# Optimization experiments

Measured on AMD Instinct MI355X. Metric: run time of the kernel, lower is better.

The kernel has to match this reference:

```python
import jax, jax.numpy as jnp
import numpy as np

L, D = 8192, 1024


def binary_operator_diag(q_i, q_j):
    # elementwise (diagonal) linear-recurrence combine: h_j = A_j * h_i + b_j
    A_i, b_i = q_i
    A_j, b_j = q_j
    return A_j * A_i, A_j * b_i + b_j


def setup_inputs() -> dict:
    key = jax.random.key(0)
    k_in, k_u, k_th, k_bre, k_bim = jax.random.split(key, 5)
    inputs = jax.random.normal(k_in, (L, D), dtype=jnp.float32)
    # stable LRU init: |lambda| = exp(-exp(nu)) = sqrt(u), u in (0.01, 0.99)
    u = jax.random.uniform(k_u, (D,), jnp.float32, 0.01, 0.99)
    nu = jnp.log(-0.5 * jnp.log(u))
    # phase stored in log-space (forward uses exp(theta))
    theta = jnp.log(jax.random.uniform(k_th, (D,), jnp.float32, 1e-3, 6.28))
    gamma_log = 0.5 * jnp.log(1.0 - u)  # = log(sqrt(1 - |lambda|^2))
    norm = np.float32(np.sqrt(2.0 * D))
    B_re = jax.random.normal(k_bre, (D, D), jnp.float32) / norm
    B_im = jax.random.normal(k_bim, (D, D), jnp.float32) / norm
    return {"inputs": inputs, "theta": theta, "nu": nu,
            "gamma_log": gamma_log, "B_re": B_re, "B_im": B_im}


def reference(inputs, theta, nu, gamma_log, B_re, B_im):
    # diagonal transition: lambda = exp(-exp(nu) + i*exp(theta)), shape [D]
    diag_lambda = jnp.exp(-jnp.exp(nu) + 1j * jnp.exp(theta))
    # normalized input matrix: (B_re + i B_im) * exp(gamma_log)[:, None]
    B_norm = (B_re + 1j * B_im) * jnp.exp(gamma_log)[:, None]  # [D, D] complex
    # Bu[t] = B_norm @ u_t  -> batched as one GEMM: [L, D] complex
    Bu = jnp.einsum('ld,kd->lk', inputs.astype(B_norm.dtype), B_norm)
    Lambda_elements = jnp.broadcast_to(diag_lambda[None, :], Bu.shape)
    # parallel associative scan over time (axis 0), elementwise over channels
    _, hidden_states = jax.lax.associative_scan(
        binary_operator_diag, (Lambda_elements, Bu))
    return hidden_states.real + inputs
```

## Files before the change

kernel.cpp:

```cpp
#include <hip/hip_runtime.h>
#include <cstdint>
#include <cstddef>

typedef float  f32x4   __attribute__((ext_vector_type(4)));
typedef short  bf16x8  __attribute__((ext_vector_type(8)));
typedef unsigned short u16x8 __attribute__((ext_vector_type(8)));

#define L_SEQ   8192
#define D_DIM   1024
#define N_COL   2048
#define N_PAIR  512
#define CHUNK_T 16
#define N_CHUNK 512

__device__ __forceinline__ unsigned short f2bf(float f) {
  unsigned int b = __float_as_uint(f);
  b += 0x7FFFu + ((b >> 16) & 1u);
  return (unsigned short)(b >> 16);
}
__device__ __forceinline__ float bf2f(unsigned short u) {
  return __uint_as_float((unsigned int)u << 16);
}
__device__ __forceinline__ void gload_lds16(const void* g, void* lds) {
  __builtin_amdgcn_global_load_lds(
      (const __attribute__((address_space(1))) void*)g,
      (__attribute__((address_space(3))) void*)lds, 16, 0, 0);
}
__device__ __forceinline__ float2 cmul(float2 a, float2 b) {
  return make_float2(a.x * b.x - a.y * b.y, a.x * b.y + a.y * b.x);
}
__device__ __forceinline__ float2 csqr(float2 a) {
  return make_float2(a.x * a.x - a.y * a.y, 2.f * a.x * a.y);
}
__device__ __forceinline__ void cfma2(const float4& lm, float2& h0, float2& h1,
                                      const float4& v) {
  float nr0 = fmaf(lm.x, h0.x, fmaf(-lm.y, h0.y, v.x));
  float ni0 = fmaf(lm.x, h0.y, fmaf(lm.y, h0.x, v.y));
  float nr1 = fmaf(lm.z, h1.x, fmaf(-lm.w, h1.y, v.z));
  float ni1 = fmaf(lm.z, h1.y, fmaf(lm.w, h1.x, v.w));
  h0.x = nr0; h0.y = ni0; h1.x = nr1; h1.y = ni1;
}

__global__ __launch_bounds__(256) void k_prep(
    const float* __restrict__ in, const float* __restrict__ Bre,
    const float* __restrict__ Bim, const float* __restrict__ gamma_log,
    const float* __restrict__ theta, const float* __restrict__ nu,
    unsigned short* __restrict__ A, unsigned short* __restrict__ W,
    float2* __restrict__ lam) {
  int b = blockIdx.x;
  if (b < 4096) {
    int i = b * 256 + threadIdx.x;
    const float4* p = (const float4*)in;
    float4 a = p[2 * i], c = p[2 * i + 1];
    u16x8 o;
    o[0] = f2bf(a.x); o[1] = f2bf(a.y); o[2] = f2bf(a.z); o[3] = f2bf(a.w);
    o[4] = f2bf(c.x); o[5] = f2bf(c.y); o[6] = f2bf(c.z); o[7] = f2bf(c.w);
    *(u16x8*)(A + (size_t)i * 8) = o;
  } else if (b < 5120) {
    int t = (b - 4096) * 256 + threadIdx.x;
    int row = t >> 7;
    int seg = t & 127;
    int k = row >> 1;
    const float* src = (row & 1) ? Bim : Bre;
    float g = expf(gamma_log[k]);
    const float4* p = (const float4*)(src + (size_t)k * D_DIM + seg * 8);
    float4 a = p[0], c = p[1];
    u16x8 o;
    o[0] = f2bf(a.x * g); o[1] = f2bf(a.y * g); o[2] = f2bf(a.z * g); o[3] = f2bf(a.w * g);
    o[4] = f2bf(c.x * g); o[5] = f2bf(c.y * g); o[6] = f2bf(c.z * g); o[7] = f2bf(c.w * g);
    *(u16x8*)(W + (size_t)row * D_DIM + seg * 8) = o;
  } else {
    int k = (b - 5120) * 256 + threadIdx.x;
    if (k < D_DIM) {
      float mod = expf(-expf(nu[k]));
      float ang = expf(theta[k]);
      lam[k] = make_float2(mod * cosf(ang), mod * sinf(ang));
    }
  }
}

__global__ __launch_bounds__(512, 1) void k_gemm(const unsigned short* __restrict__ A,
                                                 const unsigned short* __restrict__ W,
                                                 unsigned short* __restrict__ Bu16,
                                                 float2* __restrict__ agg2,
                                                 const float2* __restrict__ lam) {
  extern __shared__ char smem[];

  const int tid = threadIdx.x;
  const int l = tid & 63, w = tid >> 6;
  const int wm = w >> 2, wn = w & 3;

  int orig = blockIdx.x;
  int wgid = (orig & 7) * 32 + (orig >> 3);
  const int mt = wgid >> 3, nt = wgid & 7;
  const size_t m0 = (size_t)mt * 256, n0 = (size_t)nt * 256;

  const int srow = tid >> 3;
  const int scs  = tid & 7;
  const int cA   = scs ^ (srow & 7);
  const size_t srcoff0 = (size_t)srow * 2048 + (size_t)cA * 16;
  const size_t srcoff1 = srcoff0 + 64 * 2048;
  const int dst0 = tid * 16, dst1 = 8192 + tid * 16;

#define STAGE(Mptr, Mbase, Msel, bb, hh, TT) do {                                   \
    const char* s_ = (const char*)(Mptr) +                                          \
        (((Mbase) + (size_t)(hh) * 128) * 2048 + (size_t)(TT) * 128);               \
    char* d_ = smem + (Msel) * 65536 + (bb) * 32768 + (hh) * 16384;                 \
    gload_lds16(s_ + srcoff0, d_ + dst0);                                           \
    gload_lds16(s_ + srcoff1, d_ + dst1);                                           \
  } while (0)

  int aroff[8], broff[4];
#pragma unroll
  for (int fr = 0; fr < 8; ++fr) {
    int lrow = fr * 32 + wm * 16 + (l & 15);
    aroff[fr] = (lrow >> 7) * 16384 + (lrow & 127) * 128;
  }
#pragma unroll
  for (int fn = 0; fn < 4; ++fn) {
    int lrow = fn * 64 + wn * 16 + (l & 15);
    broff[fn] = (lrow >> 7) * 16384 + (lrow & 127) * 128;
  }
  const int swk0 = (((l >> 4)) ^ (l & 7)) << 4;
  const int swk1 = ((4 + (l >> 4)) ^ (l & 7)) << 4;

  f32x4 acc[8][4];
#pragma unroll
  for (int m = 0; m < 8; ++m)
#pragma unroll
    for (int n = 0; n < 4; ++n) acc[m][n] = (f32x4){0.f, 0.f, 0.f, 0.f};

  bf16x8 af[4][2], bfr[4][2];

#define LGKMC0 asm volatile("s_waitcnt lgkmcnt(0)" ::: "memory")
#define VMCNT4 asm volatile("s_waitcnt vmcnt(4)" ::: "memory")
#define VMCNT0 asm volatile("s_waitcnt vmcnt(0)" ::: "memory")
#define BAR()  do { asm volatile("" ::: "memory"); __builtin_amdgcn_s_barrier(); \
                    asm volatile("" ::: "memory"); } while (0)

  STAGE(W, n0, 1, 0, 0, 0);
  STAGE(A, m0, 0, 0, 1, 0);
  STAGE(A, m0, 0, 0, 0, 0);
  STAGE(W, n0, 1, 0, 1, 0);
  STAGE(W, n0, 1, 1, 0, 1);
  STAGE(A, m0, 0, 1, 1, 1);
  VMCNT4;
  BAR();

  for (int kt = 0; kt < 16; ++kt) {
    const int buf = kt & 1;
    const int abase = buf * 32768;
    const int bbase = 65536 + buf * 32768;
    const int b1 = (kt + 1) & 1, b2 = kt & 1;
    const bool s1 = (kt + 1 < 16), s2 = (kt + 2 < 16);

#pragma unroll
    for (int i = 0; i < 4; ++i) {
      af[i][0] = *(const bf16x8*)(smem + abase + aroff[i] + swk0);
      af[i][1] = *(const bf16x8*)(smem + abase + aroff[i] + swk1);
    }
#pragma unroll
    for (int fn = 0; fn < 2; ++fn) {
      bfr[fn][0] = *(const bf16x8*)(smem + bbase + broff[fn] + swk0);
      bfr[fn][1] = *(const bf16x8*)(smem + bbase + broff[fn] + swk1);
    }
    if (s1) STAGE(A, m0, 0, b1, 0, kt + 1);
    BAR();
    LGKMC0;
    __builtin_amdgcn_s_setprio(1);
#pragma unroll
    for (int i = 0; i < 4; ++i)
#pragma unroll
      for (int fn = 0; fn < 2; ++fn) {
        acc[i][fn] = __builtin_amdgcn_mfma_f32_16x16x32_bf16(af[i][0], bfr[fn][0], acc[i][fn], 0, 0, 0);
        acc[i][fn] = __builtin_amdgcn_mfma_f32_16x16x32_bf16(af[i][1], bfr[fn][1], acc[i][fn], 0, 0, 0);
      }
    __builtin_amdgcn_s_setprio(0);
    BAR();

#pragma unroll
    for (int fn = 2; fn < 4; ++fn) {
      bfr[fn][0] = *(const bf16x8*)(smem + bbase + broff[fn] + swk0);
      bfr[fn][1] = *(const bf16x8*)(smem + bbase + broff[fn] + swk1);
    }
    if (s1) STAGE(W, n0, 1, b1, 1, kt + 1);
    BAR();
    LGKMC0;
    __builtin_amdgcn_s_setprio(1);
#pragma unroll
    for (int i = 0; i < 4; ++i)
#pragma unroll
      for (int fn = 2; fn < 4; ++fn) {
        acc[i][fn] = __builtin_amdgcn_mfma_f32_16x16x32_bf16(af[i][0], bfr[fn][0], acc[i][fn], 0, 0, 0);
        acc[i][fn] = __builtin_amdgcn_mfma_f32_16x16x32_bf16(af[i][1], bfr[fn][1], acc[i][fn], 0, 0, 0);
      }
    __builtin_amdgcn_s_setprio(0);
    BAR();

#pragma unroll
    for (int i = 0; i < 4; ++i) {
      af[i][0] = *(const bf16x8*)(smem + abase + aroff[4 + i] + swk0);
      af[i][1] = *(const bf16x8*)(smem + abase + aroff[4 + i] + swk1);
    }
    if (s2) STAGE(W, n0, 1, b2, 0, kt + 2);
    BAR();
    LGKMC0;
    __builtin_amdgcn_s_setprio(1);
#pragma unroll
    for (int i = 0; i < 4; ++i)
#pragma unroll
      for (int fn = 2; fn < 4; ++fn) {
        acc[4 + i][fn] = __builtin_amdgcn_mfma_f32_16x16x32_bf16(af[i][0], bfr[fn][0], acc[4 + i][fn], 0, 0, 0);
        acc[4 + i][fn] = __builtin_amdgcn_mfma_f32_16x16x32_bf16(af[i][1], bfr[fn][1], acc[4 + i][fn], 0, 0, 0);
      }
    __builtin_amdgcn_s_setprio(0);
    BAR();

    if (s2) STAGE(A, m0, 0, b2, 1, kt + 2);
    __builtin_amdgcn_s_setprio(1);
#pragma unroll
    for (int i = 0; i < 4; ++i)
#pragma unroll
      for (int fn = 0; fn < 2; ++fn) {
        acc[4 + i][fn] = __builtin_amdgcn_mfma_f32_16x16x32_bf16(af[i][0], bfr[fn][0], acc[4 + i][fn], 0, 0, 0);
        acc[4 + i][fn] = __builtin_amdgcn_mfma_f32_16x16x32_bf16(af[i][1], bfr[fn][1], acc[4 + i][fn], 0, 0, 0);
      }
    __builtin_amdgcn_s_setprio(0);
    if (kt < 14) VMCNT4; else VMCNT0;
    BAR();
  }
#undef STAGE

#pragma unroll
  for (int fr = 0; fr < 8; ++fr)
#pragma unroll
    for (int fn = 0; fn < 4; ++fn) {
      int col = fn * 64 + wn * 16 + (l & 15);
#pragma unroll
      for (int j = 0; j < 4; ++j) {
        int row = fr * 32 + wm * 16 + (l >> 4) * 4 + j;
        int byte = row * 512 + ((col * 2) ^ ((row & 7) << 4));
        *(unsigned short*)(smem + byte) = f2bf(acc[fr][fn][j]);
      }
    }
  __syncthreads();

  {
    unsigned short* gbase = Bu16 + m0 * N_COL + n0;
#pragma unroll
    for (int pass = 0; pass < 16; ++pass) {
      int row = pass * 16 + (tid >> 5);
      int c = tid & 31;
      int byte = row * 512 + ((c * 16) ^ ((row & 7) << 4));
      f32x4 v = *(const f32x4*)(smem + byte);
      *(f32x4*)(gbase + (size_t)row * N_COL + c * 8) = v;
    }
  }

#pragma unroll
  for (int i = 0; i < 4; ++i) {
    int q = i * 512 + tid;
    int c = q >> 7, ch = q & 127;
    float2 lmv = lam[(n0 >> 1) + ch];
    unsigned int pr[16];
#pragma unroll
    for (int s = 0; s < 16; ++s) {
      int row = c * 16 + s;
      pr[s] = *(const unsigned int*)(smem + row * 512 + ((ch * 4) ^ ((row & 7) << 4)));
    }
    float2 h = {0.f, 0.f};
#pragma unroll
    for (int s = 0; s < 16; ++s) {
      float br = bf2f((unsigned short)(pr[s] & 0xFFFFu));
      float bi = bf2f((unsigned short)(pr[s] >> 16));
      float nr = fmaf(lmv.x, h.x, fmaf(-lmv.y, h.y, br));
      float ni = fmaf(lmv.x, h.y, fmaf(lmv.y, h.x, bi));
      h.x = nr; h.y = ni;
    }
    agg2[(size_t)(mt * 16 + c) * 1024 + (n0 >> 1) + ch] = h;
  }
}

__global__ __launch_bounds__(256) void k_scan2(const float4* __restrict__ agg4,
                                               const float4* __restrict__ lam4,
                                               float4* __restrict__ carry4) {
  int wave = blockIdx.x * 4 + (threadIdx.x >> 6);
  int lane = threadIdx.x & 63;
  int j = wave;
  float4 lm = lam4[j];
  float2 lT0 = {lm.x, lm.y}, lT1 = {lm.z, lm.w};
#pragma unroll
  for (int i = 0; i < 4; ++i) { lT0 = csqr(lT0); lT1 = csqr(lT1); }

  float4 a[8];
  float2 T0 = {0.f, 0.f}, T1 = {0.f, 0.f};
  float4 lTv = make_float4(lT0.x, lT0.y, lT1.x, lT1.y);
#pragma unroll
  for (int i = 0; i < 8; ++i) {
    a[i] = agg4[(size_t)(lane * 8 + i) * N_PAIR + j];
    cfma2(lTv, T0, T1, a[i]);
  }

  float2 M0 = lT0, M1 = lT1;
#pragma unroll
  for (int i = 0; i < 3; ++i) { M0 = csqr(M0); M1 = csqr(M1); }
  float2 S0 = T0, S1 = T1;
#pragma unroll
  for (int d = 1; d < 64; d <<= 1) {
    float2 u0, u1;
    u0.x = __shfl_up(S0.x, d); u0.y = __shfl_up(S0.y, d);
    u1.x = __shfl_up(S1.x, d); u1.y = __shfl_up(S1.y, d);
    if (lane >= d) {
      float2 m0 = cmul(M0, u0), m1 = cmul(M1, u1);
      S0.x += m0.x; S0.y += m0.y; S1.x += m1.x; S1.y += m1.y;
    }
    M0 = csqr(M0); M1 = csqr(M1);
  }
  float2 P0, P1;
  P0.x = __shfl_up(S0.x, 1); P0.y = __shfl_up(S0.y, 1);
  P1.x = __shfl_up(S1.x, 1); P1.y = __shfl_up(S1.y, 1);
  if (lane == 0) { P0 = make_float2(0.f, 0.f); P1 = make_float2(0.f, 0.f); }

#pragma unroll
  for (int i = 0; i < 8; ++i) {
    carry4[(size_t)(lane * 8 + i) * N_PAIR + j] = make_float4(P0.x, P0.y, P1.x, P1.y);
    cfma2(lTv, P0, P1, a[i]);
  }
}

__global__ __launch_bounds__(256) void k_scan3(const u16x8* __restrict__ Bu8,
                                               const float4* __restrict__ lam4,
                                               const float4* __restrict__ carry4,
                                               const ushort4* __restrict__ inA,
                                               float4* __restrict__ out4) {
  int t = blockIdx.x * 256 + threadIdx.x;
  int c = t >> 8, q = t & 255;
  float4 lm0 = lam4[2 * q], lm1 = lam4[2 * q + 1];
  float4 cv0 = carry4[(size_t)c * N_PAIR + 2 * q];
  float4 cv1 = carry4[(size_t)c * N_PAIR + 2 * q + 1];
  float2 h0 = {cv0.x, cv0.y}, h1 = {cv0.z, cv0.w};
  float2 h2 = {cv1.x, cv1.y}, h3 = {cv1.z, cv1.w};
#pragma unroll
  for (int s = 0; s < CHUNK_T; ++s) {
    size_t row = (size_t)c * CHUNK_T + s;
    u16x8 b = Bu8[row * 256 + q];
    float4 v0 = make_float4(bf2f(b[0]), bf2f(b[1]), bf2f(b[2]), bf2f(b[3]));
    float4 v1 = make_float4(bf2f(b[4]), bf2f(b[5]), bf2f(b[6]), bf2f(b[7]));
    cfma2(lm0, h0, h1, v0);
    cfma2(lm1, h2, h3, v1);
    ushort4 iv = inA[row * 256 + q];
    out4[row * 256 + q] = make_float4(h0.x + bf2f(iv.x), h1.x + bf2f(iv.y),
                                      h2.x + bf2f(iv.z), h3.x + bf2f(iv.w));
  }
}

extern "C" void kernel_launch(void* const* d_in, const int* in_sizes, int n_in,
                              void* d_out, int out_size, void* d_ws, size_t ws_size,
                              hipStream_t stream) {
  (void)in_sizes; (void)n_in; (void)out_size; (void)ws_size;
  const float* inputs    = (const float*)d_in[0];
  const float* theta     = (const float*)d_in[1];
  const float* nu        = (const float*)d_in[2];
  const float* gamma_log = (const float*)d_in[3];
  const float* Bre       = (const float*)d_in[4];
  const float* Bim       = (const float*)d_in[5];

  char* ws = (char*)d_ws;
  float2*         lam   = (float2*)ws;
  unsigned short* A     = (unsigned short*)(ws + (1 << 16));
  unsigned short* W     = (unsigned short*)(ws + (1 << 16) + (16u << 20));
  unsigned short* Bu16  = (unsigned short*)(ws + (1 << 16) + (20u << 20));
  float2*         agg   = (float2*)(ws + (1 << 16) + (52u << 20));
  float4*         carry = (float4*)(ws + (1 << 16) + (56u << 20));

  hipFuncSetAttribute((const void*)k_gemm,
                      hipFuncAttributeMaxDynamicSharedMemorySize, 131072);

  k_prep<<<5124, 256, 0, stream>>>(inputs, Bre, Bim, gamma_log, theta, nu, A, W, lam);
  k_gemm<<<256, 512, 131072, stream>>>(A, W, Bu16, agg, (const float2*)lam);
  k_scan2<<<N_PAIR / 4, 256, 0, stream>>>((const float4*)agg, (const float4*)lam, carry);
  k_scan3<<<(N_CHUNK * 256) / 256, 256, 0, stream>>>((const u16x8*)Bu16,
                                                     (const float4*)lam, carry,
                                                     (const ushort4*)A,
                                                     (float4*)d_out);
}
```

Before: 69.87 us.

## Fuse GEMM, chunk-carry scan, and final scan into one cooperative kernel

Merges the GEMM, the cross-chunk carry scan, and the final per-chunk scan into a single cooperative kernel that uses two grid-wide syncs. The Bu tile stays in LDS, so the bf16 Bu round-trip through global memory and two kernel launches go away. The cost is two grid barriers, only 2 of the 8 waves per block doing work during the carry scan, and output writes strided per channel that are less coalesced than the old float4 stores. It also depends on all 256 blocks being co-resident, one per CU.

```diff
diff --git a/kernel.cpp b/kernel.cpp
--- a/kernel.cpp
+++ b/kernel.cpp
@@ -1,6 +1,9 @@
 #include <hip/hip_runtime.h>
+#include <hip/hip_cooperative_groups.h>
 #include <cstdint>
 #include <cstddef>
+
+namespace cg = cooperative_groups;
 
 typedef float  f32x4   __attribute__((ext_vector_type(4)));
 typedef short  bf16x8  __attribute__((ext_vector_type(8)));
@@ -9,7 +12,6 @@
 #define L_SEQ   8192
 #define D_DIM   1024
 #define N_COL   2048
-#define N_PAIR  512
 #define CHUNK_T 16
 #define N_CHUNK 512
 
@@ -79,11 +81,12 @@
   }
 }
 
-__global__ __launch_bounds__(512, 1) void k_gemm(const unsigned short* __restrict__ A,
-                                                 const unsigned short* __restrict__ W,
-                                                 unsigned short* __restrict__ Bu16,
-                                                 float2* __restrict__ agg2,
-                                                 const float2* __restrict__ lam) {
+__global__ __launch_bounds__(512, 1) void k_fused(const unsigned short* __restrict__ A,
+                                                  const unsigned short* __restrict__ W,
+                                                  float* __restrict__ out,
+                                                  float2* __restrict__ agg2,
+                                                  float2* __restrict__ carry2,
+                                                  const float2* __restrict__ lam) {
   extern __shared__ char smem[];
 
   const int tid = threadIdx.x;
@@ -245,18 +248,6 @@
     }
   __syncthreads();
 
-  {
-    unsigned short* gbase = Bu16 + m0 * N_COL + n0;
-#pragma unroll
-    for (int pass = 0; pass < 16; ++pass) {
-      int row = pass * 16 + (tid >> 5);
-      int c = tid & 31;
-      int byte = row * 512 + ((c * 16) ^ ((row & 7) << 4));
-      f32x4 v = *(const f32x4*)(smem + byte);
-      *(f32x4*)(gbase + (size_t)row * N_COL + c * 8) = v;
-    }
-  }
-
 #pragma unroll
   for (int i = 0; i < 4; ++i) {
     int q = i * 512 + tid;
@@ -279,78 +270,80 @@
     }
     agg2[(size_t)(mt * 16 + c) * 1024 + (n0 >> 1) + ch] = h;
   }
-}
-
-__global__ __launch_bounds__(256) void k_scan2(const float4* __restrict__ agg4,
-                                               const float4* __restrict__ lam4,
-                                               float4* __restrict__ carry4) {
-  int wave = blockIdx.x * 4 + (threadIdx.x >> 6);
-  int lane = threadIdx.x & 63;
-  int j = wave;
-  float4 lm = lam4[j];
-  float2 lT0 = {lm.x, lm.y}, lT1 = {lm.z, lm.w};
-#pragma unroll
-  for (int i = 0; i < 4; ++i) { lT0 = csqr(lT0); lT1 = csqr(lT1); }
-
-  float4 a[8];
-  float2 T0 = {0.f, 0.f}, T1 = {0.f, 0.f};
-  float4 lTv = make_float4(lT0.x, lT0.y, lT1.x, lT1.y);
-#pragma unroll
-  for (int i = 0; i < 8; ++i) {
-    a[i] = agg4[(size_t)(lane * 8 + i) * N_PAIR + j];
-    cfma2(lTv, T0, T1, a[i]);
-  }
-
-  float2 M0 = lT0, M1 = lT1;
-#pragma unroll
-  for (int i = 0; i < 3; ++i) { M0 = csqr(M0); M1 = csqr(M1); }
-  float2 S0 = T0, S1 = T1;
-#pragma unroll
-  for (int d = 1; d < 64; d <<= 1) {
-    float2 u0, u1;
-    u0.x = __shfl_up(S0.x, d); u0.y = __shfl_up(S0.y, d);
-    u1.x = __shfl_up(S1.x, d); u1.y = __shfl_up(S1.y, d);
-    if (lane >= d) {
-      float2 m0 = cmul(M0, u0), m1 = cmul(M1, u1);
-      S0.x += m0.x; S0.y += m0.y; S1.x += m1.x; S1.y += m1.y;
-    }
-    M0 = csqr(M0); M1 = csqr(M1);
-  }
-  float2 P0, P1;
-  P0.x = __shfl_up(S0.x, 1); P0.y = __shfl_up(S0.y, 1);
-  P1.x = __shfl_up(S1.x, 1); P1.y = __shfl_up(S1.y, 1);
-  if (lane == 0) { P0 = make_float2(0.f, 0.f); P1 = make_float2(0.f, 0.f); }
-
-#pragma unroll
-  for (int i = 0; i < 8; ++i) {
-    carry4[(size_t)(lane * 8 + i) * N_PAIR + j] = make_float4(P0.x, P0.y, P1.x, P1.y);
-    cfma2(lTv, P0, P1, a[i]);
-  }
-}
-
-__global__ __launch_bounds__(256) void k_scan3(const u16x8* __restrict__ Bu8,
-                                               const float4* __restrict__ lam4,
-                                               const float4* __restrict__ carry4,
-                                               const ushort4* __restrict__ inA,
-                                               float4* __restrict__ out4) {
-  int t = blockIdx.x * 256 + threadIdx.x;
-  int c = t >> 8, q = t & 255;
-  float4 lm0 = lam4[2 * q], lm1 = lam4[2 * q + 1];
-  float4 cv0 = carry4[(size_t)c * N_PAIR + 2 * q];
-  float4 cv1 = carry4[(size_t)c * N_PAIR + 2 * q + 1];
-  float2 h0 = {cv0.x, cv0.y}, h1 = {cv0.z, cv0.w};
-  float2 h2 = {cv1.x, cv1.y}, h3 = {cv1.z, cv1.w};
-#pragma unroll
-  for (int s = 0; s < CHUNK_T; ++s) {
-    size_t row = (size_t)c * CHUNK_T + s;
-    u16x8 b = Bu8[row * 256 + q];
-    float4 v0 = make_float4(bf2f(b[0]), bf2f(b[1]), bf2f(b[2]), bf2f(b[3]));
-    float4 v1 = make_float4(bf2f(b[4]), bf2f(b[5]), bf2f(b[6]), bf2f(b[7]));
-    cfma2(lm0, h0, h1, v0);
-    cfma2(lm1, h2, h3, v1);
-    ushort4 iv = inA[row * 256 + q];
-    out4[row * 256 + q] = make_float4(h0.x + bf2f(iv.x), h1.x + bf2f(iv.y),
-                                      h2.x + bf2f(iv.z), h3.x + bf2f(iv.w));
+
+  cg::this_grid().sync();
+
+  if (w < 2) {
+    int j = orig * 2 + w;
+    const float4* agg4 = (const float4*)agg2;
+    float4* carry4 = (float4*)carry2;
+    float4 lm4 = ((const float4*)lam)[j];
+    float2 lT0 = {lm4.x, lm4.y}, lT1 = {lm4.z, lm4.w};
+#pragma unroll
+    for (int i = 0; i < 4; ++i) { lT0 = csqr(lT0); lT1 = csqr(lT1); }
+    float4 lTv = make_float4(lT0.x, lT0.y, lT1.x, lT1.y);
+
+    float4 a[8];
+    float2 T0 = {0.f, 0.f}, T1 = {0.f, 0.f};
+#pragma unroll
+    for (int i = 0; i < 8; ++i) {
+      a[i] = agg4[(size_t)(l * 8 + i) * 512 + j];
+      cfma2(lTv, T0, T1, a[i]);
+    }
+    float2 M0 = lT0, M1 = lT1;
+#pragma unroll
+    for (int i = 0; i < 3; ++i) { M0 = csqr(M0); M1 = csqr(M1); }
+    float2 S0 = T0, S1 = T1;
+#pragma unroll
+    for (int d = 1; d < 64; d <<= 1) {
+      float2 u0, u1;
+      u0.x = __shfl_up(S0.x, d); u0.y = __shfl_up(S0.y, d);
+      u1.x = __shfl_up(S1.x, d); u1.y = __shfl_up(S1.y, d);
+      if (l >= d) {
+        float2 q0 = cmul(M0, u0), q1 = cmul(M1, u1);
+        S0.x += q0.x; S0.y += q0.y; S1.x += q1.x; S1.y += q1.y;
+      }
+      M0 = csqr(M0); M1 = csqr(M1);
+    }
+    float2 P0, P1;
+    P0.x = __shfl_up(S0.x, 1); P0.y = __shfl_up(S0.y, 1);
+    P1.x = __shfl_up(S1.x, 1); P1.y = __shfl_up(S1.y, 1);
+    if (l == 0) { P0 = make_float2(0.f, 0.f); P1 = make_float2(0.f, 0.f); }
+#pragma unroll
+    for (int i = 0; i < 8; ++i) {
+      carry4[(size_t)(l * 8 + i) * 512 + j] = make_float4(P0.x, P0.y, P1.x, P1.y);
+      cfma2(lTv, P0, P1, a[i]);
+    }
+  }
+
+  cg::this_grid().sync();
+
+#pragma unroll
+  for (int i = 0; i < 4; ++i) {
+    int q = i * 512 + tid;
+    int c = q >> 7, ch = q & 127;
+    float2 lmv = lam[(n0 >> 1) + ch];
+    float2 h = carry2[(size_t)(mt * 16 + c) * 1024 + (n0 >> 1) + ch];
+    unsigned int pr[16];
+#pragma unroll
+    for (int s = 0; s < 16; ++s) {
+      int row = c * 16 + s;
+      pr[s] = *(const unsigned int*)(smem + row * 512 + ((ch * 4) ^ ((row & 7) << 4)));
+    }
+    unsigned short av[16];
+#pragma unroll
+    for (int s = 0; s < 16; ++s)
+      av[s] = A[(m0 + (size_t)c * 16 + s) * 1024 + (n0 >> 1) + ch];
+    float* op = out + (m0 + (size_t)c * 16) * 1024 + (n0 >> 1) + ch;
+#pragma unroll
+    for (int s = 0; s < 16; ++s) {
+      float br = bf2f((unsigned short)(pr[s] & 0xFFFFu));
+      float bi = bf2f((unsigned short)(pr[s] >> 16));
+      float nr = fmaf(lmv.x, h.x, fmaf(-lmv.y, h.y, br));
+      float ni = fmaf(lmv.x, h.y, fmaf(lmv.y, h.x, bi));
+      h.x = nr; h.y = ni;
+      op[(size_t)s * 1024] = h.x + bf2f(av[s]);
+    }
   }
 }
 
@@ -369,18 +362,17 @@
   float2*         lam   = (float2*)ws;
   unsigned short* A     = (unsigned short*)(ws + (1 << 16));
   unsigned short* W     = (unsigned short*)(ws + (1 << 16) + (16u << 20));
-  unsigned short* Bu16  = (unsigned short*)(ws + (1 << 16) + (20u << 20));
-  float2*         agg   = (float2*)(ws + (1 << 16) + (52u << 20));
-  float4*         carry = (float4*)(ws + (1 << 16) + (56u << 20));
-
-  hipFuncSetAttribute((const void*)k_gemm,
+  float2*         agg   = (float2*)(ws + (1 << 16) + (20u << 20));
+  float2*         carry = (float2*)(ws + (1 << 16) + (24u << 20));
+  float*          out   = (float*)d_out;
+
+  hipFuncSetAttribute((const void*)k_fused,
                       hipFuncAttributeMaxDynamicSharedMemorySize, 131072);
 
   k_prep<<<5124, 256, 0, stream>>>(inputs, Bre, Bim, gamma_log, theta, nu, A, W, lam);
-  k_gemm<<<256, 512, 131072, stream>>>(A, W, Bu16, agg, (const float2*)lam);
-  k_scan2<<<N_PAIR / 4, 256, 0, stream>>>((const float4*)agg, (const float4*)lam, carry);
-  k_scan3<<<(N_CHUNK * 256) / 256, 256, 0, stream>>>((const u16x8*)Bu16,
-                                                     (const float4*)lam, carry,
-                                                     (const ushort4*)A,
-                                                     (float4*)d_out);
-}
+
+  void* args[] = {(void*)&A, (void*)&W, (void*)&out, (void*)&agg, (void*)&carry,
+                  (void*)&lam};
+  hipLaunchCooperativeKernel((const void*)k_fused, dim3(256), dim3(512), args,
+                             131072, stream);
+}
```

After: 129.6 us. 85.5% more time.

## Software-pipeline LDS fragment loads across MFMA phases, drop extra barriers

Applied to the files above, without the earlier changes.

Restructures the GEMM main loop so the LDS fragment reads for the next phase, and for the next k-tile, are issued before the MFMA block that consumes the previous fragments. This overlaps LDS latency with matrix math. It also removes the explicit lgkmcnt waits and several barriers per iteration, and reorders the quadrant schedule and the vmcnt thresholds to match. In exchange it raises register pressure from the extra fragment buffers and depends on delicate ordering of LDS reads against async global-to-LDS writes.

```diff
diff --git a/kernel.cpp b/kernel.cpp
--- a/kernel.cpp
+++ b/kernel.cpp
@@ -130,103 +130,112 @@
 #pragma unroll
     for (int n = 0; n < 4; ++n) acc[m][n] = (f32x4){0.f, 0.f, 0.f, 0.f};
 
-  bf16x8 af[4][2], bfr[4][2];
-
-#define LGKMC0 asm volatile("s_waitcnt lgkmcnt(0)" ::: "memory")
+  bf16x8 a03[4][2], a47[4][2], b01[2][2], b23[2][2];
+
+#define VMCNT2 asm volatile("s_waitcnt vmcnt(2)" ::: "memory")
 #define VMCNT4 asm volatile("s_waitcnt vmcnt(4)" ::: "memory")
 #define VMCNT0 asm volatile("s_waitcnt vmcnt(0)" ::: "memory")
 #define BAR()  do { asm volatile("" ::: "memory"); __builtin_amdgcn_s_barrier(); \
                     asm volatile("" ::: "memory"); } while (0)
 
+  STAGE(A, m0, 0, 0, 0, 0);
   STAGE(W, n0, 1, 0, 0, 0);
   STAGE(A, m0, 0, 0, 1, 0);
-  STAGE(A, m0, 0, 0, 0, 0);
   STAGE(W, n0, 1, 0, 1, 0);
   STAGE(W, n0, 1, 1, 0, 1);
   STAGE(A, m0, 0, 1, 1, 1);
   VMCNT4;
   BAR();
+#pragma unroll
+  for (int i = 0; i < 4; ++i) {
+    a03[i][0] = *(const bf16x8*)(smem + aroff[i] + swk0);
+    a03[i][1] = *(const bf16x8*)(smem + aroff[i] + swk1);
+  }
+#pragma unroll
+  for (int fn = 0; fn < 2; ++fn) {
+    b01[fn][0] = *(const bf16x8*)(smem + 65536 + broff[fn] + swk0);
+    b01[fn][1] = *(const bf16x8*)(smem + 65536 + broff[fn] + swk1);
+  }
 
   for (int kt = 0; kt < 16; ++kt) {
     const int buf = kt & 1;
     const int abase = buf * 32768;
     const int bbase = 65536 + buf * 32768;
-    const int b1 = (kt + 1) & 1, b2 = kt & 1;
+    const int nbuf = (kt + 1) & 1;
+    const int b1 = nbuf, b2 = buf;
     const bool s1 = (kt + 1 < 16), s2 = (kt + 2 < 16);
 
 #pragma unroll
-    for (int i = 0; i < 4; ++i) {
-      af[i][0] = *(const bf16x8*)(smem + abase + aroff[i] + swk0);
-      af[i][1] = *(const bf16x8*)(smem + abase + aroff[i] + swk1);
-    }
-#pragma unroll
     for (int fn = 0; fn < 2; ++fn) {
-      bfr[fn][0] = *(const bf16x8*)(smem + bbase + broff[fn] + swk0);
-      bfr[fn][1] = *(const bf16x8*)(smem + bbase + broff[fn] + swk1);
+      b23[fn][0] = *(const bf16x8*)(smem + bbase + broff[2 + fn] + swk0);
+      b23[fn][1] = *(const bf16x8*)(smem + bbase + broff[2 + fn] + swk1);
     }
     if (s1) STAGE(A, m0, 0, b1, 0, kt + 1);
-    BAR();
-    LGKMC0;
     __builtin_amdgcn_s_setprio(1);
 #pragma unroll
     for (int i = 0; i < 4; ++i)
 #pragma unroll
       for (int fn = 0; fn < 2; ++fn) {
-        acc[i][fn] = __builtin_amdgcn_mfma_f32_16x16x32_bf16(af[i][0], bfr[fn][0], acc[i][fn], 0, 0, 0);
-        acc[i][fn] = __builtin_amdgcn_mfma_f32_16x16x32_bf16(af[i][1], bfr[fn][1], acc[i][fn], 0, 0, 0);
+        acc[i][fn] = __builtin_amdgcn_mfma_f32_16x16x32_bf16(a03[i][0], b01[fn][0], acc[i][fn], 0, 0, 0);
+        acc[i][fn] = __builtin_amdgcn_mfma_f32_16x16x32_bf16(a03[i][1], b01[fn][1], acc[i][fn], 0, 0, 0);
       }
     __builtin_amdgcn_s_setprio(0);
     BAR();
 
 #pragma unroll
-    for (int fn = 2; fn < 4; ++fn) {
-      bfr[fn][0] = *(const bf16x8*)(smem + bbase + broff[fn] + swk0);
-      bfr[fn][1] = *(const bf16x8*)(smem + bbase + broff[fn] + swk1);
+    for (int i = 0; i < 4; ++i) {
+      a47[i][0] = *(const bf16x8*)(smem + abase + aroff[4 + i] + swk0);
+      a47[i][1] = *(const bf16x8*)(smem + abase + aroff[4 + i] + swk1);
     }
     if (s1) STAGE(W, n0, 1, b1, 1, kt + 1);
-    BAR();
-    LGKMC0;
     __builtin_amdgcn_s_setprio(1);
 #pragma unroll
     for (int i = 0; i < 4; ++i)
 #pragma unroll
-      for (int fn = 2; fn < 4; ++fn) {
-        acc[i][fn] = __builtin_amdgcn_mfma_f32_16x16x32_bf16(af[i][0], bfr[fn][0], acc[i][fn], 0, 0, 0);
-        acc[i][fn] = __builtin_amdgcn_mfma_f32_16x16x32_bf16(af[i][1], bfr[fn][1], acc[i][fn], 0, 0, 0);
+      for (int fn = 0; fn < 2; ++fn) {
+        acc[i][2 + fn] = __builtin_amdgcn_mfma_f32_16x16x32_bf16(a03[i][0], b23[fn][0], acc[i][2 + fn], 0, 0, 0);
+        acc[i][2 + fn] = __builtin_amdgcn_mfma_f32_16x16x32_bf16(a03[i][1], b23[fn][1], acc[i][2 + fn], 0, 0, 0);
       }
     __builtin_amdgcn_s_setprio(0);
     BAR();
 
-#pragma unroll
-    for (int i = 0; i < 4; ++i) {
-      af[i][0] = *(const bf16x8*)(smem + abase + aroff[4 + i] + swk0);
-      af[i][1] = *(const bf16x8*)(smem + abase + aroff[4 + i] + swk1);
-    }
     if (s2) STAGE(W, n0, 1, b2, 0, kt + 2);
+    __builtin_amdgcn_s_setprio(1);
+#pragma unroll
+    for (int i = 0; i < 4; ++i)
+#pragma unroll
+      for (int fn = 0; fn < 2; ++fn) {
+        acc[4 + i][2 + fn] = __builtin_amdgcn_mfma_f32_16x16x32_bf16(a47[i][0], b23[fn][0], acc[4 + i][2 + fn], 0, 0, 0);
+        acc[4 + i][2 + fn] = __builtin_amdgcn_mfma_f32_16x16x32_bf16(a47[i][1], b23[fn][1], acc[4 + i][2 + fn], 0, 0, 0);
+      }
+    __builtin_amdgcn_s_setprio(0);
+    if (kt < 14) VMCNT2; else VMCNT0;
     BAR();
-    LGKMC0;
+
     __builtin_amdgcn_s_setprio(1);
 #pragma unroll
     for (int i = 0; i < 4; ++i)
 #pragma unroll
-      for (int fn = 2; fn < 4; ++fn) {
-        acc[4 + i][fn] = __builtin_amdgcn_mfma_f32_16x16x32_bf16(af[i][0], bfr[fn][0], acc[4 + i][fn], 0, 0, 0);
-        acc[4 + i][fn] = __builtin_amdgcn_mfma_f32_16x16x32_bf16(af[i][1], bfr[fn][1], acc[4 + i][fn], 0, 0, 0);
+      for (int fn = 0; fn < 2; ++fn) {
+        acc[4 + i][fn] = __builtin_amdgcn_mfma_f32_16x16x32_bf16(a47[i][0], b01[fn][0], acc[4 + i][fn], 0, 0, 0);
+        acc[4 + i][fn] = __builtin_amdgcn_mfma_f32_16x16x32_bf16(a47[i][1], b01[fn][1], acc[4 + i][fn], 0, 0, 0);
       }
     __builtin_amdgcn_s_setprio(0);
-    BAR();
-
+    if (s1) {
+      const int nab = nbuf * 32768;
+      const int nbb = 65536 + nbuf * 32768;
+#pragma unroll
+      for (int i = 0; i < 4; ++i) {
+        a03[i][0] = *(const bf16x8*)(smem + nab + aroff[i] + swk0);
+        a03[i][1] = *(const bf16x8*)(smem + nab + aroff[i] + swk1);
+      }
+#pragma unroll
+      for (int fn = 0; fn < 2; ++fn) {
+        b01[fn][0] = *(const bf16x8*)(smem + nbb + broff[fn] + swk0);
+        b01[fn][1] = *(const bf16x8*)(smem + nbb + broff[fn] + swk1);
+      }
+    }
     if (s2) STAGE(A, m0, 0, b2, 1, kt + 2);
-    __builtin_amdgcn_s_setprio(1);
-#pragma unroll
-    for (int i = 0; i < 4; ++i)
-#pragma unroll
-      for (int fn = 0; fn < 2; ++fn) {
-        acc[4 + i][fn] = __builtin_amdgcn_mfma_f32_16x16x32_bf16(af[i][0], bfr[fn][0], acc[4 + i][fn], 0, 0, 0);
-        acc[4 + i][fn] = __builtin_amdgcn_mfma_f32_16x16x32_bf16(af[i][1], bfr[fn][1], acc[4 + i][fn], 0, 0, 0);
-      }
-    __builtin_amdgcn_s_setprio(0);
-    if (kt < 14) VMCNT4; else VMCNT0;
     BAR();
   }
 #undef STAGE
```

New measurement: 69.77 us. About the same (-0.1%).
